# Performance work log

Hardware: AMD Instinct MI355X
Metric: run time of the kernel (lower is better)

Reference implementation:

```python
import jax, jax.numpy as jnp
import numpy as np

T, B, DZ, DH, DS = 1000, 256, 64, 256, 16


def setup_inputs() -> dict:
    key = jax.random.key(0)
    k = jax.random.split(key, 6)
    r_w1 = 1.0 / np.sqrt(DZ)   # init_uniform_same: r = 1/sqrt(last dim)
    r_w2 = 1.0 / np.sqrt(DH)
    r_c = 1.0 / np.sqrt(DS)
    # W_trial=True: same initial matrix repeated across trials
    W1 = jnp.tile(jax.random.uniform(k[0], (DH, DZ), minval=-r_w1, maxval=r_w1), (B, 1, 1))
    W2 = jnp.tile(jax.random.uniform(k[1], (DZ, DH), minval=-r_w2, maxval=r_w2), (B, 1, 1))
    C = jax.random.uniform(k[2], (DZ, DS), minval=-r_c, maxval=r_c)
    A = jnp.full((DZ,), 0.95, dtype=jnp.float32)
    h1 = jax.random.normal(k[3], (DH,), dtype=jnp.float32)
    h2 = jax.random.normal(k[4], (DZ,), dtype=jnp.float32)
    kz, ks = jax.random.split(k[5])
    z0 = jax.random.normal(kz, (B, DZ), dtype=jnp.float32)
    s = jax.random.normal(ks, (T, B, DS), dtype=jnp.float32) * 0.1
    return {"z0": z0, "s": s, "A": A, "W1": W1, "W2": W2, "h1": h1, "h2": h2, "C": C}


def reference(z0, s, A, W1, W2, h1, h2, C):
    # Precompute external-input projection for all steps: s_t @ C.T  -> [T, B, DZ]
    Cs = jnp.einsum('tbs,zs->tbz', s, C)

    def step(z, cs_t):
        # per-trial W1: Wz = einsum('ij,ijk->ik', z, W1^T) == einsum('bj,bhj->bh', z, W1)
        Wz = jnp.einsum('bj,bhj->bh', z, W1)                       # [B, DH]
        z_act = jax.nn.relu(Wz + h1) - jax.nn.relu(Wz)             # clipped shPLRNN nonlinearity
        z_new = A * z + jnp.einsum('bh,bzh->bz', z_act, W2) + h2 + cs_t
        return z_new, z_new

    _, z_seq = jax.lax.scan(step, z0, Cs)  # z_seq: [T, B, DZ]
    return z_seq
```

## Files before the change

kernel.cpp:

```cpp
#include <hip/hip_runtime.h>

#define T_STEPS 1000
#define NB 256
#define DZ 64
#define DH 256
#define DS 16
#define CHUNK 32
#define NCHUNK 32

__device__ __forceinline__ void barrier_lgkm() {
    asm volatile("s_waitcnt lgkmcnt(0)\n\ts_barrier" ::: "memory");
}

template<int CTRL>
__device__ __forceinline__ float dpp_add(float x) {
    int y = __builtin_amdgcn_update_dpp(0, __float_as_int(x), CTRL, 0xF, 0xF, true);
    return x + __int_as_float(y);
}
__device__ __forceinline__ float row16_allsum(float x) {
    x = dpp_add<0x128>(x);
    x = dpp_add<0x124>(x);
    x = dpp_add<0x122>(x);
    x = dpp_add<0x121>(x);
    return x;
}

__global__ __launch_bounds__(512)
__attribute__((amdgpu_waves_per_eu(2, 2)))
void plrnn_scan(const float* __restrict__ z0, const float* __restrict__ s,
                const float* __restrict__ A,  const float* __restrict__ W1,
                const float* __restrict__ W2, const float* __restrict__ h1,
                const float* __restrict__ h2, const float* __restrict__ C,
                float* __restrict__ out)
{
    const int tid  = threadIdx.x;
    const int b    = blockIdx.x;
    const int w    = tid >> 6;
    const int l    = tid & 63;
    const int h    = tid >> 1;
    const int half = tid & 1;
    const int R    = (w << 2) | (l >> 4);
    const int r4   = l & 15;
    const int j0   = 2 * R;
    const int j1   = 2 * R + 1;

    __shared__ __align__(16) float z_sh[DZ];
    __shared__ __align__(16) float za_sh[320];
    __shared__ __align__(16) float s_sh[CHUNK * DS];

    float4 w1v[8];
    {
        const float4* p = (const float4*)(W1 + (size_t)b * DH * DZ + (size_t)h * DZ + half * 32);
        #pragma unroll
        for (int k = 0; k < 8; ++k) w1v[k] = p[k];
    }
    float4 w2a[4];
    float4 w2b[4];
    {
        const float4* p0 = (const float4*)(W2 + (size_t)b * DZ * DH + (size_t)j0 * DH + 16 * r4);
        const float4* p1 = (const float4*)(W2 + (size_t)b * DZ * DH + (size_t)j1 * DH + 16 * r4);
        #pragma unroll
        for (int k = 0; k < 4; ++k) { w2a[k] = p0[k]; w2b[k] = p1[k]; }
    }
    const float c0  = C[j0 * DS + r4];
    const float c1  = C[j1 * DS + r4];
    const float h1r = h1[h];
    const float A0  = A[j0],  A1  = A[j1];
    const float h20 = h2[j0], h21 = h2[j1];
    float zr0 = z0[b * DZ + j0];
    float zr1 = z0[b * DZ + j1];

    if (tid < DZ) z_sh[tid] = z0[b * DZ + tid];

    const int srow = tid >> 4, scol = tid & 15;
    float sreg = s[(size_t)min(srow, T_STEPS - 1) * NB * DS + (size_t)b * DS + scol];

    const int zi = h + ((h >> 4) << 2);

    __syncthreads();

    for (int ci = 0; ci < NCHUNK; ++ci) {
        const int t0 = ci * CHUNK;
        s_sh[tid] = sreg;
        {
            int tl = min(t0 + CHUNK + srow, T_STEPS - 1);
            sreg = s[(size_t)tl * NB * DS + (size_t)b * DS + scol];
        }

        for (int tt = 0; tt < CHUNK; ++tt) {
            const float4* z4 = (const float4*)(z_sh + half * 32);
            float a0 = 0.f, a1 = 0.f, a2 = 0.f, a3 = 0.f;
            #pragma unroll
            for (int k = 0; k < 8; ++k) {
                float4 zv = z4[k];
                a0 = fmaf(w1v[k].x, zv.x, a0);
                a1 = fmaf(w1v[k].y, zv.y, a1);
                a2 = fmaf(w1v[k].z, zv.z, a2);
                a3 = fmaf(w1v[k].w, zv.w, a3);
            }
            float p1 = (a0 + a1) + (a2 + a3);
            p1 = dpp_add<0xB1>(p1);
            float za = fmaxf(p1 + h1r, 0.f) - fmaxf(p1, 0.f);
            if (half == 0) za_sh[zi] = za;
            barrier_lgkm();

            const float4* q4 = (const float4*)(za_sh + 20 * r4);
            float sv = s_sh[tt * DS + r4];
            float p00 = c0 * sv, p01 = 0.f, p02 = 0.f, p03 = 0.f;
            float p10 = c1 * sv, p11 = 0.f, p12 = 0.f, p13 = 0.f;
            #pragma unroll
            for (int k = 0; k < 4; ++k) {
                float4 v = q4[k];
                p00 = fmaf(w2a[k].x, v.x, p00);
                p01 = fmaf(w2a[k].y, v.y, p01);
                p02 = fmaf(w2a[k].z, v.z, p02);
                p03 = fmaf(w2a[k].w, v.w, p03);
                p10 = fmaf(w2b[k].x, v.x, p10);
                p11 = fmaf(w2b[k].y, v.y, p11);
                p12 = fmaf(w2b[k].z, v.z, p12);
                p13 = fmaf(w2b[k].w, v.w, p13);
            }
            float pa = (p00 + p01) + (p02 + p03);
            float pb = (p10 + p11) + (p12 + p13);
            pa = row16_allsum(pa);
            pb = row16_allsum(pb);

            float zn0 = fmaf(A0, zr0, pa + h20);
            float zn1 = fmaf(A1, zr1, pb + h21);
            zr0 = zn0; zr1 = zn1;
            const int t = t0 + tt;
            if (r4 < 2) {
                float zsel = (r4 == 0) ? zn0 : zn1;
                z_sh[j0 + r4] = zsel;
                if (t < T_STEPS)
                    out[(size_t)t * NB * DZ + (size_t)b * DZ + j0 + r4] = zsel;
            }
            barrier_lgkm();
        }
    }
}

extern "C" void kernel_launch(void* const* d_in, const int* in_sizes, int n_in,
                              void* d_out, int out_size, void* d_ws, size_t ws_size,
                              hipStream_t stream) {
    const float* z0p = (const float*)d_in[0];
    const float* sp  = (const float*)d_in[1];
    const float* Ap  = (const float*)d_in[2];
    const float* W1p = (const float*)d_in[3];
    const float* W2p = (const float*)d_in[4];
    const float* h1p = (const float*)d_in[5];
    const float* h2p = (const float*)d_in[6];
    const float* Cp  = (const float*)d_in[7];

    plrnn_scan<<<dim3(NB), dim3(512), 0, stream>>>(z0p, sp, Ap, W1p, W2p, h1p, h2p, Cp,
                                                   (float*)d_out);
}
```

Baseline: 637.6 us.

## Double threads per block to halve per-thread work in each recurrence step

Moves from 512 to 1024 threads per block. Each hidden unit's W1 dot product is now split across four lanes, combined with an extra DPP quad swap, and each thread owns a single output row of W2 instead of two. This shortens the serial FMA chain per time step, which is the critical path of the latency-bound scan. The s-chunk size grows to 64 to match the thread count, and the inner time loop is unrolled by 4. In exchange, each step's two barriers now synchronize 16 waves instead of 8, and register budget per thread is tighter.

```diff
diff --git a/kernel.cpp b/kernel.cpp
--- a/kernel.cpp
+++ b/kernel.cpp
@@ -5,8 +5,8 @@
 #define DZ 64
 #define DH 256
 #define DS 16
-#define CHUNK 32
-#define NCHUNK 32
+#define CHUNK 64
+#define NCHUNK 16
 
 __device__ __forceinline__ void barrier_lgkm() {
     asm volatile("s_waitcnt lgkmcnt(0)\n\ts_barrier" ::: "memory");
@@ -25,50 +25,42 @@
     return x;
 }
 
-__global__ __launch_bounds__(512)
-__attribute__((amdgpu_waves_per_eu(2, 2)))
+__global__ __launch_bounds__(1024)
+__attribute__((amdgpu_waves_per_eu(4, 4)))
 void plrnn_scan(const float* __restrict__ z0, const float* __restrict__ s,
                 const float* __restrict__ A,  const float* __restrict__ W1,
                 const float* __restrict__ W2, const float* __restrict__ h1,
                 const float* __restrict__ h2, const float* __restrict__ C,
                 float* __restrict__ out)
 {
-    const int tid  = threadIdx.x;
-    const int b    = blockIdx.x;
-    const int w    = tid >> 6;
-    const int l    = tid & 63;
-    const int h    = tid >> 1;
-    const int half = tid & 1;
-    const int R    = (w << 2) | (l >> 4);
-    const int r4   = l & 15;
-    const int j0   = 2 * R;
-    const int j1   = 2 * R + 1;
+    const int tid = threadIdx.x;
+    const int b   = blockIdx.x;
+    const int h   = tid >> 2;
+    const int q   = tid & 3;
+    const int j   = tid >> 4;
+    const int r4  = tid & 15;
 
     __shared__ __align__(16) float z_sh[DZ];
     __shared__ __align__(16) float za_sh[320];
     __shared__ __align__(16) float s_sh[CHUNK * DS];
 
-    float4 w1v[8];
+    float4 w1v[4];
     {
-        const float4* p = (const float4*)(W1 + (size_t)b * DH * DZ + (size_t)h * DZ + half * 32);
+        const float4* p = (const float4*)(W1 + (size_t)b * DH * DZ) + 4 * tid;
         #pragma unroll
-        for (int k = 0; k < 8; ++k) w1v[k] = p[k];
+        for (int k = 0; k < 4; ++k) w1v[k] = p[k];
     }
-    float4 w2a[4];
-    float4 w2b[4];
+    float4 w2v[4];
     {
-        const float4* p0 = (const float4*)(W2 + (size_t)b * DZ * DH + (size_t)j0 * DH + 16 * r4);
-        const float4* p1 = (const float4*)(W2 + (size_t)b * DZ * DH + (size_t)j1 * DH + 16 * r4);
+        const float4* p = (const float4*)(W2 + (size_t)b * DZ * DH) + 4 * tid;
         #pragma unroll
-        for (int k = 0; k < 4; ++k) { w2a[k] = p0[k]; w2b[k] = p1[k]; }
+        for (int k = 0; k < 4; ++k) w2v[k] = p[k];
     }
-    const float c0  = C[j0 * DS + r4];
-    const float c1  = C[j1 * DS + r4];
+    const float cj  = C[tid];
     const float h1r = h1[h];
-    const float A0  = A[j0],  A1  = A[j1];
-    const float h20 = h2[j0], h21 = h2[j1];
-    float zr0 = z0[b * DZ + j0];
-    float zr1 = z0[b * DZ + j1];
+    const float Aj  = A[j];
+    const float h2j = h2[j];
+    float zr = z0[b * DZ + j];
 
     if (tid < DZ) z_sh[tid] = z0[b * DZ + tid];
 
@@ -76,6 +68,7 @@
     float sreg = s[(size_t)min(srow, T_STEPS - 1) * NB * DS + (size_t)b * DS + scol];
 
     const int zi = h + ((h >> 4) << 2);
+    float* outp = out + (size_t)b * DZ + j;
 
     __syncthreads();
 
@@ -87,11 +80,12 @@
             sreg = s[(size_t)tl * NB * DS + (size_t)b * DS + scol];
         }
 
+        #pragma unroll 4
         for (int tt = 0; tt < CHUNK; ++tt) {
-            const float4* z4 = (const float4*)(z_sh + half * 32);
+            const float4* z4 = (const float4*)(z_sh + 16 * q);
             float a0 = 0.f, a1 = 0.f, a2 = 0.f, a3 = 0.f;
             #pragma unroll
-            for (int k = 0; k < 8; ++k) {
+            for (int k = 0; k < 4; ++k) {
                 float4 zv = z4[k];
                 a0 = fmaf(w1v[k].x, zv.x, a0);
                 a1 = fmaf(w1v[k].y, zv.y, a1);
@@ -100,41 +94,33 @@
             }
             float p1 = (a0 + a1) + (a2 + a3);
             p1 = dpp_add<0xB1>(p1);
+            p1 = dpp_add<0x4E>(p1);
             float za = fmaxf(p1 + h1r, 0.f) - fmaxf(p1, 0.f);
-            if (half == 0) za_sh[zi] = za;
+            if (q == 0) za_sh[zi] = za;
             barrier_lgkm();
 
             const float4* q4 = (const float4*)(za_sh + 20 * r4);
             float sv = s_sh[tt * DS + r4];
-            float p00 = c0 * sv, p01 = 0.f, p02 = 0.f, p03 = 0.f;
-            float p10 = c1 * sv, p11 = 0.f, p12 = 0.f, p13 = 0.f;
+            float p00 = cj * sv, p01 = 0.f, p02 = 0.f, p03 = 0.f;
             #pragma unroll
             for (int k = 0; k < 4; ++k) {
                 float4 v = q4[k];
-                p00 = fmaf(w2a[k].x, v.x, p00);
-                p01 = fmaf(w2a[k].y, v.y, p01);
-                p02 = fmaf(w2a[k].z, v.z, p02);
-                p03 = fmaf(w2a[k].w, v.w, p03);
-                p10 = fmaf(w2b[k].x, v.x, p10);
-                p11 = fmaf(w2b[k].y, v.y, p11);
-                p12 = fmaf(w2b[k].z, v.z, p12);
-                p13 = fmaf(w2b[k].w, v.w, p13);
+                p00 = fmaf(w2v[k].x, v.x, p00);
+                p01 = fmaf(w2v[k].y, v.y, p01);
+                p02 = fmaf(w2v[k].z, v.z, p02);
+                p03 = fmaf(w2v[k].w, v.w, p03);
             }
             float pa = (p00 + p01) + (p02 + p03);
-            float pb = (p10 + p11) + (p12 + p13);
             pa = row16_allsum(pa);
-            pb = row16_allsum(pb);
 
-            float zn0 = fmaf(A0, zr0, pa + h20);
-            float zn1 = fmaf(A1, zr1, pb + h21);
-            zr0 = zn0; zr1 = zn1;
+            float zn = fmaf(Aj, zr, pa + h2j);
+            zr = zn;
             const int t = t0 + tt;
-            if (r4 < 2) {
-                float zsel = (r4 == 0) ? zn0 : zn1;
-                z_sh[j0 + r4] = zsel;
-                if (t < T_STEPS)
-                    out[(size_t)t * NB * DZ + (size_t)b * DZ + j0 + r4] = zsel;
+            if (r4 == 0) {
+                z_sh[j] = zn;
+                if (t < T_STEPS) *outp = zn;
             }
+            outp += NB * DZ;
             barrier_lgkm();
         }
     }
@@ -152,6 +138,6 @@
     const float* h2p = (const float*)d_in[6];
     const float* Cp  = (const float*)d_in[7];
 
-    plrnn_scan<<<dim3(NB), dim3(512), 0, stream>>>(z0p, sp, Ap, W1p, W2p, h1p, h2p, Cp,
-                                                   (float*)d_out);
+    plrnn_scan<<<dim3(NB), dim3(1024), 0, stream>>>(z0p, sp, Ap, W1p, W2p, h1p, h2p, Cp,
+                                                    (float*)d_out);
 }
```

New measurement: 593.3 us. 1.07x faster.
